# Kernel optimization log

Measured on AMD Instinct MI355X. Metric: run time of the kernel, lower is better.

Reference implementation:

```python
import jax, jax.numpy as jnp
import numpy as np

B, T, H, I = 128, 1024, 512, 64
DT, TAU, NOISE_VAR = 1.0, 10.0, 0.1


def setup_inputs() -> dict:
    key = jax.random.key(0)
    k1, k2, k3, k4 = jax.random.split(key, 4)
    x = jax.random.normal(k1, (B, T, I), dtype=jnp.float32)
    # W_in: rows have unit-ish norm in the original init; normal/sqrt(I) is equivalent scale
    W_in = jax.random.normal(k2, (H, I), dtype=jnp.float32) / np.float32(np.sqrt(I))
    # W_hidden: randn/sqrt(H) then spectral-radius normalized; /sqrt(H) gives radius ~1
    W_hidden = jax.random.normal(k3, (H, H), dtype=jnp.float32) / np.float32(np.sqrt(H))
    # noise drawn inside forward in the original; materialized here: N(0, noise_var)
    sigma = jax.random.normal(k4, (H, T, B), dtype=jnp.float32) * np.float32(NOISE_VAR)
    h0 = jnp.zeros((H, B), dtype=jnp.float32)
    return {"x": x, "W_in": W_in, "W_hidden": W_hidden, "sigma": sigma, "h0": h0}


def reference(x, W_in, W_hidden, sigma, h0):
    c1 = jnp.float32(1.0 - DT / TAU)
    c2 = jnp.float32(DT / TAU)
    # precomputed input projection: [T, H, B] (scan carries over leading T axis)
    w_input = jnp.einsum("hi,bti->thb", W_in, x)
    sig = jnp.transpose(sigma, (1, 0, 2))  # [T, H, B]

    def step(h, inp):
        w_in_t, s_t = inp
        w_h = W_hidden @ jax.nn.sigmoid(h)          # [H, B]
        h_new = c1 * h + c2 * (w_in_t + w_h + s_t)  # leaky integration
        return h_new, h_new.T                        # emit [B, H]

    h_last, out_tbh = jax.lax.scan(step, h0, (w_input, sig))
    out = jnp.transpose(out_tbh, (1, 0, 2))  # [B, T, H]
    return out, h_last
```

## Files before the change

### kernel.cpp

```cpp
#include <hip/hip_runtime.h>
#include <stdint.h>

#define B_  128
#define T_  1024
#define H_  512
#define I_  64
#define TB_ 131072

typedef _Float16 half2_t __attribute__((ext_vector_type(2)));

union U32H2 { uint32_t u; half2_t h; };
union U16H  { uint16_t u; _Float16 h; };

static __device__ __forceinline__ half2_t u2h(uint32_t u){ U32H2 x; x.u=u; return x.h; }
static __device__ __forceinline__ uint32_t h2u(half2_t h){ U32H2 x; x.h=h; return x.u; }

#if defined(__has_builtin)
#if __has_builtin(__builtin_amdgcn_fdot2)
#define HAVE_FDOT2 1
#endif
#endif

static __device__ __forceinline__ float fdot2f(half2_t a, half2_t b, float c){
#ifdef HAVE_FDOT2
    return __builtin_amdgcn_fdot2(a, b, c, false);
#else
    return c + (float)a[0]*(float)b[0] + (float)a[1]*(float)b[1];
#endif
}

#define BARRIER_NODRAIN() do {                                        \
    __asm__ __volatile__("s_waitcnt lgkmcnt(0)" ::: "memory");        \
    __builtin_amdgcn_s_barrier();                                     \
    __asm__ __volatile__("" ::: "memory");                            \
} while (0)

__global__ __launch_bounds__(256) void k_wingemm(const float* __restrict__ x,
                                                 const float* __restrict__ Win,
                                                 const float* __restrict__ sigma,
                                                 uint32_t* __restrict__ r2)
{
    __shared__ float As[128*65];
    __shared__ float Ws[64*65];
    const int t   = blockIdx.x;
    const int j0  = blockIdx.y * 64;
    const int tid = threadIdx.x;

#pragma unroll
    for (int k = 0; k < 8; k++){
        int qid = k*256 + tid;
        int row = qid >> 4;
        int qq  = qid & 15;
        float4 v = *(const float4*)(x + ((size_t)row*T_ + t)*I_ + qq*4);
        float* d = As + row*65 + qq*4;
        d[0]=v.x; d[1]=v.y; d[2]=v.z; d[3]=v.w;
    }
#pragma unroll
    for (int k = 0; k < 4; k++){
        int qid = k*256 + tid;
        int row = qid >> 4;
        int qq  = qid & 15;
        float4 v = *(const float4*)(Win + (size_t)(j0+row)*I_ + qq*4);
        float* d = Ws + row*65 + qq*4;
        d[0]=v.x; d[1]=v.y; d[2]=v.z; d[3]=v.w;
    }
    __syncthreads();

    const int tj = tid & 15;
    const int tb = tid >> 4;

    float acc[8][2][2];
#pragma unroll
    for (int bb=0; bb<8; bb++)
#pragma unroll
        for (int jj=0; jj<2; jj++){ acc[bb][jj][0]=0.f; acc[bb][jj][1]=0.f; }

#pragma unroll 4
    for (int i = 0; i < 64; i++){
        float a[8];
#pragma unroll
        for (int bb=0; bb<8; bb++) a[bb] = As[(tb + 16*bb)*65 + i];
        float wv[2][2];
#pragma unroll
        for (int jj=0; jj<2; jj++){
            wv[jj][0] = Ws[(2*tj + 32*jj    )*65 + i];
            wv[jj][1] = Ws[(2*tj + 32*jj + 1)*65 + i];
        }
#pragma unroll
        for (int bb=0; bb<8; bb++)
#pragma unroll
            for (int jj=0; jj<2; jj++){
                acc[bb][jj][0] += a[bb]*wv[jj][0];
                acc[bb][jj][1] += a[bb]*wv[jj][1];
            }
    }
    __syncthreads();

    float* Sg = As;
#pragma unroll
    for (int k = 0; k < 8; k++){
        int qid = k*256 + tid;
        int row = qid >> 5;
        int qq  = qid & 31;
        float4 v = *(const float4*)(sigma + (size_t)(j0+row)*TB_ + (size_t)t*128 + qq*4);
        float* d = Sg + row*130 + qq*4;
        d[0]=v.x; d[1]=v.y; d[2]=v.z; d[3]=v.w;
    }
    __syncthreads();

#pragma unroll
    for (int bb=0; bb<8; bb++){
        int bcol = tb + 16*bb;
        int mi = t*128 + bcol;
#pragma unroll
        for (int jj=0; jj<2; jj++){
            int jA = 2*tj + 32*jj;
            float a0 = acc[bb][jj][0] + Sg[(jA    )*130 + bcol];
            float a1 = acc[bb][jj][1] + Sg[(jA + 1)*130 + bcol];
            half2_t hv; hv[0]=(_Float16)a0; hv[1]=(_Float16)a1;
            r2[(size_t)mi*256 + (j0>>1) + tj + 16*jj] = h2u(hv);
        }
    }
}

__global__ __launch_bounds__(512, 2) void k_rnn(const float* __restrict__ Wh,
                                                const float* __restrict__ Win,
                                                const float* __restrict__ x,
                                                const float* __restrict__ sigma,
                                                const float* __restrict__ h0,
                                                const uint16_t* __restrict__ r16,
                                                float* __restrict__ out,
                                                int use_r)
{
    extern __shared__ char smem[];
    uint32_t*  WL  = (uint32_t*)smem;
    float*     par = (float*)(smem + 131072);
    _Float16*  sb  = (_Float16*)(smem + 131072 + 18432);

    const int b = blockIdx.x;
    const int t = threadIdx.x;
    const int w = t >> 6;
    const int l = t & 63;
    const int j = t;
    const int phase = (l & 15) << 2;

    half2_t wreg[6][32];
#pragma unroll
    for (int m = 0; m < 8; m++){
        const int row = l + 64*m;
        const float4* wr = (const float4*)(Wh + (size_t)row*H_ + (w << 6));
#pragma unroll
        for (int q = 0; q < 16; q++){
            float4 v = wr[q];
            half2_t a; a[0]=(_Float16)v.x; a[1]=(_Float16)v.y;
            half2_t c; c[0]=(_Float16)v.z; c[1]=(_Float16)v.w;
            int pp = 2*q;
            if (m < 6){
                wreg[m][pp]   = a;
                wreg[m][pp+1] = c;
            } else {
                int base = (m-6)*32;
                WL[t*64 + ((base + pp     + phase) & 63)] = h2u(a);
                WL[t*64 + ((base + pp + 1 + phase) & 63)] = h2u(c);
            }
        }
    }

    float h = h0[(size_t)j*B_ + b];
    const uint32_t* WLt = WL + t*64;
    const uint32_t* sbu = (const uint32_t*)sb;
    float* outp = out + (size_t)b*T_*H_ + j;
    const uint16_t* rp = r16 + (size_t)b*H_ + j;

    for (int ts = 0; ts < T_; ts++){
        uint16_t ru = 0;
        if (use_r) ru = rp[(size_t)ts * 65536];

        float e = __expf(-h);
        float s = 1.0f / (1.0f + e);
        sb[j] = (_Float16)s;
        BARRIER_NODRAIN();

        float p[8];
#pragma unroll
        for (int m = 0; m < 8; m++) p[m] = 0.f;

#pragma unroll
        for (int c = 0; c < 8; c++){
            uint4 sq = *(const uint4*)(sbu + (w << 5) + (c << 2));
            half2_t s0=u2h(sq.x), s1=u2h(sq.y), s2=u2h(sq.z), s3=u2h(sq.w);
            uint4 q6 = *(const uint4*)(WLt + ((4*c      + phase) & 63));
            uint4 q7 = *(const uint4*)(WLt + ((32 + 4*c + phase) & 63));
#pragma unroll
            for (int m = 0; m < 6; m++){
                p[m] = fdot2f(wreg[m][4*c+0], s0, p[m]);
                p[m] = fdot2f(wreg[m][4*c+1], s1, p[m]);
                p[m] = fdot2f(wreg[m][4*c+2], s2, p[m]);
                p[m] = fdot2f(wreg[m][4*c+3], s3, p[m]);
            }
            p[6] = fdot2f(u2h(q6.x), s0, p[6]);
            p[6] = fdot2f(u2h(q6.y), s1, p[6]);
            p[6] = fdot2f(u2h(q6.z), s2, p[6]);
            p[6] = fdot2f(u2h(q6.w), s3, p[6]);
            p[7] = fdot2f(u2h(q7.x), s0, p[7]);
            p[7] = fdot2f(u2h(q7.y), s1, p[7]);
            p[7] = fdot2f(u2h(q7.z), s2, p[7]);
            p[7] = fdot2f(u2h(q7.w), s3, p[7]);
        }

#pragma unroll
        for (int m = 0; m < 8; m++) par[(l + (m << 6))*9 + w] = p[m];
        BARRIER_NODRAIN();

        const float* pj = par + j*9;
        float P = ((pj[0] + pj[1]) + (pj[2] + pj[3]))
                + ((pj[4] + pj[5]) + (pj[6] + pj[7]));

        float rv;
        if (use_r){
            U16H cv; cv.u = ru;
            rv = (float)cv.h;
        } else {
            float acc = 0.f;
            const float4* wir = (const float4*)(Win + (size_t)j*I_);
            const float4* xr  = (const float4*)(x + ((size_t)b*T_ + ts)*I_);
#pragma unroll
            for (int q = 0; q < 16; q++){
                float4 a = wir[q]; float4 xx = xr[q];
                acc += a.x*xx.x + a.y*xx.y + a.z*xx.z + a.w*xx.w;
            }
            rv = acc + sigma[((size_t)j << 17) + (ts << 7) + b];
        }

        h = 0.9f*h + 0.1f*(P + rv);
        outp[(size_t)ts * H_] = h;
    }

    out[(size_t)B_*T_*H_ + (size_t)j*B_ + b] = h;
}

extern "C" void kernel_launch(void* const* d_in, const int* in_sizes, int n_in,
                              void* d_out, int out_size, void* d_ws, size_t ws_size,
                              hipStream_t stream)
{
    const float* x     = (const float*)d_in[0];
    const float* Win   = (const float*)d_in[1];
    const float* Wh    = (const float*)d_in[2];
    const float* sigma = (const float*)d_in[3];
    const float* h0    = (const float*)d_in[4];
    float* out = (float*)d_out;

    const size_t r_bytes = (size_t)TB_ * H_ * 2;
    const int use_r = (ws_size >= r_bytes) ? 1 : 0;

    if (use_r){
        k_wingemm<<<dim3(T_, 8), 256, 0, stream>>>(x, Win, sigma, (uint32_t*)d_ws);
    }

    const int lds_bytes = 131072 + 18432 + 1024;
    (void)hipFuncSetAttribute((const void*)k_rnn,
                              hipFuncAttributeMaxDynamicSharedMemorySize, lds_bytes);
    k_rnn<<<B_, 512, lds_bytes, stream>>>(Wh, Win, x, sigma, h0,
                                          (const uint16_t*)d_ws, out, use_r);
}
```

Before: 2.375 ms.

## Double-buffer RNN partial sums to drop a barrier, widen register weights, vectorize GEMM

```diff
diff --git a/kernel.cpp b/kernel.cpp
--- a/kernel.cpp
+++ b/kernel.cpp
@@ -40,10 +40,10 @@
                                                  const float* __restrict__ sigma,
                                                  uint32_t* __restrict__ r2)
 {
-    __shared__ float As[128*65];
-    __shared__ float Ws[64*65];
-    const int t   = blockIdx.x;
-    const int j0  = blockIdx.y * 64;
+    __shared__ float As[128*68];
+    __shared__ float Ws[64*68];
+    const int t   = blockIdx.y;
+    const int j0  = blockIdx.x * 64;
     const int tid = threadIdx.x;
 
 #pragma unroll
@@ -52,8 +52,7 @@
         int row = qid >> 4;
         int qq  = qid & 15;
         float4 v = *(const float4*)(x + ((size_t)row*T_ + t)*I_ + qq*4);
-        float* d = As + row*65 + qq*4;
-        d[0]=v.x; d[1]=v.y; d[2]=v.z; d[3]=v.w;
+        *(float4*)(As + row*68 + qq*4) = v;
     }
 #pragma unroll
     for (int k = 0; k < 4; k++){
@@ -61,8 +60,7 @@
         int row = qid >> 4;
         int qq  = qid & 15;
         float4 v = *(const float4*)(Win + (size_t)(j0+row)*I_ + qq*4);
-        float* d = Ws + row*65 + qq*4;
-        d[0]=v.x; d[1]=v.y; d[2]=v.z; d[3]=v.w;
+        *(float4*)(Ws + row*68 + qq*4) = v;
     }
     __syncthreads();
 
@@ -76,23 +74,23 @@
         for (int jj=0; jj<2; jj++){ acc[bb][jj][0]=0.f; acc[bb][jj][1]=0.f; }
 
 #pragma unroll 4
-    for (int i = 0; i < 64; i++){
-        float a[8];
-#pragma unroll
-        for (int bb=0; bb<8; bb++) a[bb] = As[(tb + 16*bb)*65 + i];
-        float wv[2][2];
-#pragma unroll
-        for (int jj=0; jj<2; jj++){
-            wv[jj][0] = Ws[(2*tj + 32*jj    )*65 + i];
-            wv[jj][1] = Ws[(2*tj + 32*jj + 1)*65 + i];
+    for (int iq = 0; iq < 16; iq++){
+        float4 w00 = *(const float4*)(Ws + (2*tj     )*68 + iq*4);
+        float4 w01 = *(const float4*)(Ws + (2*tj + 1 )*68 + iq*4);
+        float4 w10 = *(const float4*)(Ws + (2*tj + 32)*68 + iq*4);
+        float4 w11 = *(const float4*)(Ws + (2*tj + 33)*68 + iq*4);
+#pragma unroll
+        for (int bb=0; bb<8; bb++){
+            float4 a = *(const float4*)(As + (tb + 16*bb)*68 + iq*4);
+            acc[bb][0][0] += a.x*w00.x; acc[bb][0][0] += a.y*w00.y;
+            acc[bb][0][0] += a.z*w00.z; acc[bb][0][0] += a.w*w00.w;
+            acc[bb][0][1] += a.x*w01.x; acc[bb][0][1] += a.y*w01.y;
+            acc[bb][0][1] += a.z*w01.z; acc[bb][0][1] += a.w*w01.w;
+            acc[bb][1][0] += a.x*w10.x; acc[bb][1][0] += a.y*w10.y;
+            acc[bb][1][0] += a.z*w10.z; acc[bb][1][0] += a.w*w10.w;
+            acc[bb][1][1] += a.x*w11.x; acc[bb][1][1] += a.y*w11.y;
+            acc[bb][1][1] += a.z*w11.z; acc[bb][1][1] += a.w*w11.w;
         }
-#pragma unroll
-        for (int bb=0; bb<8; bb++)
-#pragma unroll
-            for (int jj=0; jj<2; jj++){
-                acc[bb][jj][0] += a[bb]*wv[jj][0];
-                acc[bb][jj][1] += a[bb]*wv[jj][1];
-            }
     }
     __syncthreads();
 
@@ -103,8 +101,7 @@
         int row = qid >> 5;
         int qq  = qid & 31;
         float4 v = *(const float4*)(sigma + (size_t)(j0+row)*TB_ + (size_t)t*128 + qq*4);
-        float* d = Sg + row*130 + qq*4;
-        d[0]=v.x; d[1]=v.y; d[2]=v.z; d[3]=v.w;
+        *(float4*)(Sg + row*130 + qq*4) = v;
     }
     __syncthreads();
 
@@ -123,117 +120,102 @@
     }
 }
 
+#define RNN_STEP(PAR, TS) {                                                   \
+    uint16_t ru = 0;                                                          \
+    if (USE_R) ru = rp[(size_t)(TS) << 16];                                   \
+    float e = __expf(-h);                                                     \
+    float s = 1.0f / (1.0f + e);                                              \
+    sb[j] = (_Float16)s;                                                      \
+    float p[8];                                                               \
+    _Pragma("unroll") for (int m = 0; m < 8; m++) p[m] = 0.f;                 \
+    _Pragma("unroll") for (int c = 0; c < 8; c++){                            \
+        uint4 sq = *(const uint4*)(sbu + (w << 5) + (c << 2));                \
+        half2_t s0=u2h(sq.x), s1=u2h(sq.y), s2=u2h(sq.z), s3=u2h(sq.w);       \
+        uint4 q7 = *(const uint4*)(WLt + ((4*c + ph) & 31));                  \
+        _Pragma("unroll") for (int m = 0; m < 7; m++){                        \
+            p[m] = fdot2f(wreg[m][4*c+0], s0, p[m]);                          \
+            p[m] = fdot2f(wreg[m][4*c+1], s1, p[m]);                          \
+            p[m] = fdot2f(wreg[m][4*c+2], s2, p[m]);                          \
+            p[m] = fdot2f(wreg[m][4*c+3], s3, p[m]);                          \
+        }                                                                     \
+        p[7] = fdot2f(u2h(q7.x), s0, p[7]);                                   \
+        p[7] = fdot2f(u2h(q7.y), s1, p[7]);                                   \
+        p[7] = fdot2f(u2h(q7.z), s2, p[7]);                                   \
+        p[7] = fdot2f(u2h(q7.w), s3, p[7]);                                   \
+    }                                                                         \
+    _Pragma("unroll") for (int m = 0; m < 8; m++)                             \
+        PAR[(l + (m << 6))*9 + w] = p[m];                                     \
+    BARRIER_NODRAIN();                                                        \
+    const float* pj = PAR + j*9;                                              \
+    float P = ((pj[0] + pj[1]) + (pj[2] + pj[3]))                             \
+            + ((pj[4] + pj[5]) + (pj[6] + pj[7]));                            \
+    float rv;                                                                 \
+    if (USE_R){ U16H cv; cv.u = ru; rv = (float)cv.h; }                       \
+    else {                                                                    \
+        float acc = 0.f;                                                      \
+        const float4* wir = (const float4*)(Win + (size_t)j*I_);              \
+        const float4* xr  = (const float4*)(x + ((size_t)b*T_ + (TS))*I_);    \
+        _Pragma("unroll") for (int q = 0; q < 16; q++){                       \
+            float4 a = wir[q]; float4 xx = xr[q];                             \
+            acc += a.x*xx.x + a.y*xx.y + a.z*xx.z + a.w*xx.w;                 \
+        }                                                                     \
+        rv = acc + sigma[((size_t)j << 17) + ((TS) << 7) + b];                \
+    }                                                                         \
+    h = 0.9f*h + 0.1f*(P + rv);                                               \
+    outp[(size_t)(TS) * H_] = h;                                              \
+}
+
+template<int USE_R>
 __global__ __launch_bounds__(512, 2) void k_rnn(const float* __restrict__ Wh,
                                                 const float* __restrict__ Win,
                                                 const float* __restrict__ x,
                                                 const float* __restrict__ sigma,
                                                 const float* __restrict__ h0,
                                                 const uint16_t* __restrict__ r16,
-                                                float* __restrict__ out,
-                                                int use_r)
+                                                float* __restrict__ out)
 {
     extern __shared__ char smem[];
-    uint32_t*  WL  = (uint32_t*)smem;
-    float*     par = (float*)(smem + 131072);
-    _Float16*  sb  = (_Float16*)(smem + 131072 + 18432);
+    uint32_t*  WL   = (uint32_t*)smem;
+    float*     parA = (float*)(smem + 65536);
+    float*     parB = (float*)(smem + 65536 + 18432);
+    _Float16*  sb   = (_Float16*)(smem + 65536 + 36864);
 
     const int b = blockIdx.x;
     const int t = threadIdx.x;
     const int w = t >> 6;
     const int l = t & 63;
     const int j = t;
-    const int phase = (l & 15) << 2;
-
-    half2_t wreg[6][32];
+    const int ph = (l & 7) << 2;
+
+    half2_t wreg[7][32];
 #pragma unroll
     for (int m = 0; m < 8; m++){
-        const int row = l + 64*m;
-        const float4* wr = (const float4*)(Wh + (size_t)row*H_ + (w << 6));
-#pragma unroll
+        const float4* wr = (const float4*)(Wh + (size_t)(l + 64*m)*H_ + (w << 6));
+#pragma unroll 2
         for (int q = 0; q < 16; q++){
             float4 v = wr[q];
             half2_t a; a[0]=(_Float16)v.x; a[1]=(_Float16)v.y;
             half2_t c; c[0]=(_Float16)v.z; c[1]=(_Float16)v.w;
             int pp = 2*q;
-            if (m < 6){
+            if (m < 7){
                 wreg[m][pp]   = a;
                 wreg[m][pp+1] = c;
             } else {
-                int base = (m-6)*32;
-                WL[t*64 + ((base + pp     + phase) & 63)] = h2u(a);
-                WL[t*64 + ((base + pp + 1 + phase) & 63)] = h2u(c);
+                WL[t*32 + ((pp     + ph) & 31)] = h2u(a);
+                WL[t*32 + ((pp + 1 + ph) & 31)] = h2u(c);
             }
         }
     }
 
     float h = h0[(size_t)j*B_ + b];
-    const uint32_t* WLt = WL + t*64;
+    const uint32_t* WLt = WL + t*32;
     const uint32_t* sbu = (const uint32_t*)sb;
     float* outp = out + (size_t)b*T_*H_ + j;
     const uint16_t* rp = r16 + (size_t)b*H_ + j;
 
-    for (int ts = 0; ts < T_; ts++){
-        uint16_t ru = 0;
-        if (use_r) ru = rp[(size_t)ts * 65536];
-
-        float e = __expf(-h);
-        float s = 1.0f / (1.0f + e);
-        sb[j] = (_Float16)s;
-        BARRIER_NODRAIN();
-
-        float p[8];
-#pragma unroll
-        for (int m = 0; m < 8; m++) p[m] = 0.f;
-
-#pragma unroll
-        for (int c = 0; c < 8; c++){
-            uint4 sq = *(const uint4*)(sbu + (w << 5) + (c << 2));
-            half2_t s0=u2h(sq.x), s1=u2h(sq.y), s2=u2h(sq.z), s3=u2h(sq.w);
-            uint4 q6 = *(const uint4*)(WLt + ((4*c      + phase) & 63));
-            uint4 q7 = *(const uint4*)(WLt + ((32 + 4*c + phase) & 63));
-#pragma unroll
-            for (int m = 0; m < 6; m++){
-                p[m] = fdot2f(wreg[m][4*c+0], s0, p[m]);
-                p[m] = fdot2f(wreg[m][4*c+1], s1, p[m]);
-                p[m] = fdot2f(wreg[m][4*c+2], s2, p[m]);
-                p[m] = fdot2f(wreg[m][4*c+3], s3, p[m]);
-            }
-            p[6] = fdot2f(u2h(q6.x), s0, p[6]);
-            p[6] = fdot2f(u2h(q6.y), s1, p[6]);
-            p[6] = fdot2f(u2h(q6.z), s2, p[6]);
-            p[6] = fdot2f(u2h(q6.w), s3, p[6]);
-            p[7] = fdot2f(u2h(q7.x), s0, p[7]);
-            p[7] = fdot2f(u2h(q7.y), s1, p[7]);
-            p[7] = fdot2f(u2h(q7.z), s2, p[7]);
-            p[7] = fdot2f(u2h(q7.w), s3, p[7]);
-        }
-
-#pragma unroll
-        for (int m = 0; m < 8; m++) par[(l + (m << 6))*9 + w] = p[m];
-        BARRIER_NODRAIN();
-
-        const float* pj = par + j*9;
-        float P = ((pj[0] + pj[1]) + (pj[2] + pj[3]))
-                + ((pj[4] + pj[5]) + (pj[6] + pj[7]));
-
-        float rv;
-        if (use_r){
-            U16H cv; cv.u = ru;
-            rv = (float)cv.h;
-        } else {
-            float acc = 0.f;
-            const float4* wir = (const float4*)(Win + (size_t)j*I_);
-            const float4* xr  = (const float4*)(x + ((size_t)b*T_ + ts)*I_);
-#pragma unroll
-            for (int q = 0; q < 16; q++){
-                float4 a = wir[q]; float4 xx = xr[q];
-                acc += a.x*xx.x + a.y*xx.y + a.z*xx.z + a.w*xx.w;
-            }
-            rv = acc + sigma[((size_t)j << 17) + (ts << 7) + b];
-        }
-
-        h = 0.9f*h + 0.1f*(P + rv);
-        outp[(size_t)ts * H_] = h;
+    for (int ts = 0; ts < T_; ts += 2){
+        RNN_STEP(parA, ts);
+        RNN_STEP(parB, ts + 1);
     }
 
     out[(size_t)B_*T_*H_ + (size_t)j*B_ + b] = h;
@@ -253,13 +235,18 @@
     const size_t r_bytes = (size_t)TB_ * H_ * 2;
     const int use_r = (ws_size >= r_bytes) ? 1 : 0;
 
+    const int lds_bytes = 65536 + 2*18432 + 1024;
+
     if (use_r){
-        k_wingemm<<<dim3(T_, 8), 256, 0, stream>>>(x, Win, sigma, (uint32_t*)d_ws);
-    }
-
-    const int lds_bytes = 131072 + 18432 + 1024;
-    (void)hipFuncSetAttribute((const void*)k_rnn,
-                              hipFuncAttributeMaxDynamicSharedMemorySize, lds_bytes);
-    k_rnn<<<B_, 512, lds_bytes, stream>>>(Wh, Win, x, sigma, h0,
-                                          (const uint16_t*)d_ws, out, use_r);
-}
+        k_wingemm<<<dim3(8, T_), 256, 0, stream>>>(x, Win, sigma, (uint32_t*)d_ws);
+        (void)hipFuncSetAttribute((const void*)(k_rnn<1>),
+                                  hipFuncAttributeMaxDynamicSharedMemorySize, lds_bytes);
+        k_rnn<1><<<B_, 512, lds_bytes, stream>>>(Wh, Win, x, sigma, h0,
+                                                 (const uint16_t*)d_ws, out);
+    } else {
+        (void)hipFuncSetAttribute((const void*)(k_rnn<0>),
+                                  hipFuncAttributeMaxDynamicSharedMemorySize, lds_bytes);
+        k_rnn<0><<<B_, 512, lds_bytes, stream>>>(Wh, Win, x, sigma, h0,
+                                                 (const uint16_t*)d_ws, out);
+    }
+}
```

Result: slower. 8.761 ms (+268.8%).
